# Kernel tuning notes

Measured on AMD Instinct MI355X. Metric: run time of the kernel, lower is better.

Reference implementation:

```python
import jax, jax.numpy as jnp
import numpy as np
from jax import lax

ALPHA = 0.99
EPS = 1e-14
B, C, T, F = 16, 2, 1000, 481


def setup_inputs() -> dict:
    key = jax.random.key(0)
    k1, _ = jax.random.split(key)
    x = jax.random.normal(k1, (B, C, T, F, 2), dtype=jnp.float32)
    init_state = jnp.ones((1, 1, F, 1), dtype=jnp.float32)
    return {"x": x, "init_state": init_state}


def reference(x, init_state):
    # complex path: x is [b, c, t, f, 2]
    b, c, t, f, _ = x.shape
    # magnitude per (b,c,t,f): sqrt(re^2 + im^2), clamped
    x_abs = jnp.sqrt(jnp.clip(jnp.sum(x * x, axis=-1, keepdims=True), EPS))  # [b,c,t,f,1]
    s0 = jnp.broadcast_to(init_state[:, :, :f], (b, c, f, 1))
    xs = jnp.moveaxis(x_abs, 2, 0)  # [t,b,c,f,1]

    def step(state, xa):
        state = xa * (1.0 - ALPHA) + state * ALPHA
        return state, state

    _, states = lax.scan(step, s0, xs)  # [t,b,c,f,1]
    states = jnp.moveaxis(states, 0, 2)  # [b,c,t,f,1]
    return x / jnp.sqrt(states)
```

## Files before the change

kernel.cpp:

```cpp
#include <hip/hip_runtime.h>


#define EPS_F 1e-14f

constexpr int B = 16, C = 2, T = 1000, F = 481;
constexpr int BC = B * C;
constexpr int FW = 64;
constexpr int NTILE = 8;
constexpr int WV = 8;
constexpr int RW = 25;
constexpr int RSTEP = WV * RW;
constexpr int NSUP = T / RSTEP;
constexpr int ROWS = F * 2;

__global__ __launch_bounds__(512, 4)
void k_fused(const float* __restrict__ x, const float* __restrict__ init_state,
             float* __restrict__ out) {
    __shared__ float lds_c[WV][FW];
    __shared__ float carry[FW];

    const int fx   = threadIdx.x & (FW - 1);
    const int w    = threadIdx.x >> 6;
    const int bc   = blockIdx.x & (BC - 1);
    const int tile = blockIdx.x >> 5;
    const int f    = tile * FW + fx;
    const bool act = (f < F);

    double p = 1.0;
    for (int i = 0; i < RW; ++i) p *= 0.99;
    const float A25 = (float)p;

    if (threadIdx.x < FW) carry[fx] = act ? init_state[f] : 1.0f;

    for (int s = 0; s < NSUP; ++s) {
        const int t0 = s * RSTEP + w * RW;
        const float* xp = x + ((size_t)(bc * T + t0) * F + f) * 2;

        float2 v[RW];
#pragma unroll
        for (int j = 0; j < RW; ++j)
            if (act) v[j] = *(const float2*)(xp + (size_t)j * ROWS);

        float Cl = 0.0f;
#pragma unroll
        for (int j = 0; j < RW; ++j)
            if (act) {
                float m = fmaxf(fmaf(v[j].x, v[j].x, v[j].y * v[j].y), EPS_F);
                Cl = fmaf(0.99f, Cl, 0.01f * __builtin_amdgcn_sqrtf(m));
            }
        lds_c[w][fx] = Cl;
        __syncthreads();

        float sloc = carry[fx];
#pragma unroll
        for (int jw = 0; jw < WV - 1; ++jw)
            if (jw < w) sloc = fmaf(A25, sloc, lds_c[jw][fx]);
        __syncthreads();

        if (w == WV - 1) carry[fx] = fmaf(A25, sloc, Cl);

        float* op = out + ((size_t)(bc * T + t0) * F + f) * 2;
#pragma unroll
        for (int j = 0; j < RW; ++j)
            if (act) {
                float m = fmaxf(fmaf(v[j].x, v[j].x, v[j].y * v[j].y), EPS_F);
                sloc = fmaf(0.99f, sloc, 0.01f * __builtin_amdgcn_sqrtf(m));
                const float inv = __builtin_amdgcn_rsqf(sloc);
                float2 o;
                o.x = v[j].x * inv;
                o.y = v[j].y * inv;
                *(float2*)(op + (size_t)j * ROWS) = o;
            }
    }
}

extern "C" void kernel_launch(void* const* d_in, const int* in_sizes, int n_in,
                              void* d_out, int out_size, void* d_ws, size_t ws_size,
                              hipStream_t stream) {
    const float* x          = (const float*)d_in[0];
    const float* init_state = (const float*)d_in[1];
    float* out = (float*)d_out;

    k_fused<<<dim3(NTILE * BC), 512, 0, stream>>>(x, init_state, out);
}
```

Baseline: 45.36 us.

## Split time scan across 16 waves in a single pass with re-read

Replaces the 5-iteration super-step loop with a single chunked scan where 16 waves each own about 62 consecutive time steps, combined via one LDS prefix using A62/A63 decay factors. Block size doubles to 1024 threads and only one barrier is needed. Inputs are no longer held in registers between the local-sum and output passes; they are re-read from memory, trading extra read traffic for fewer syncs and lower register pressure.

```diff
diff --git a/kernel.cpp b/kernel.cpp
--- a/kernel.cpp
+++ b/kernel.cpp
@@ -7,17 +7,18 @@
 constexpr int BC = B * C;
 constexpr int FW = 64;
 constexpr int NTILE = 8;
-constexpr int WV = 8;
-constexpr int RW = 25;
-constexpr int RSTEP = WV * RW;
-constexpr int NSUP = T / RSTEP;
+constexpr int WV = 16;
 constexpr int ROWS = F * 2;
 
-__global__ __launch_bounds__(512, 4)
+__device__ __forceinline__ int wbase(int w) {
+    return (w < 8) ? 63 * w : 504 + 62 * (w - 8);
+}
+__device__ __forceinline__ int wlen(int w) { return (w < 8) ? 63 : 62; }
+
+__global__ __launch_bounds__(1024, 4)
 void k_fused(const float* __restrict__ x, const float* __restrict__ init_state,
              float* __restrict__ out) {
     __shared__ float lds_c[WV][FW];
-    __shared__ float carry[FW];
 
     const int fx   = threadIdx.x & (FW - 1);
     const int w    = threadIdx.x >> 6;
@@ -27,50 +28,44 @@
     const bool act = (f < F);
 
     double p = 1.0;
-    for (int i = 0; i < RW; ++i) p *= 0.99;
-    const float A25 = (float)p;
+    for (int i = 0; i < 62; ++i) p *= 0.99;
+    const float A62 = (float)p;
+    const float A63 = (float)(p * 0.99);
 
-    if (threadIdx.x < FW) carry[fx] = act ? init_state[f] : 1.0f;
+    const int t0  = wbase(w);
+    const int len = wlen(w);
+    const float* xp = x + ((size_t)(bc * T + t0) * F + f) * 2;
 
-    for (int s = 0; s < NSUP; ++s) {
-        const int t0 = s * RSTEP + w * RW;
-        const float* xp = x + ((size_t)(bc * T + t0) * F + f) * 2;
+    float Cl = 0.0f;
+    if (act) {
+        for (int j = 0; j < len; ++j) {
+            float2 v = *(const float2*)(xp + (size_t)j * ROWS);
+            float m = fmaxf(fmaf(v.x, v.x, v.y * v.y), EPS_F);
+            Cl = fmaf(0.99f, Cl, 0.01f * __builtin_amdgcn_sqrtf(m));
+        }
+    }
+    lds_c[w][fx] = Cl;
+    __syncthreads();
 
-        float2 v[RW];
+    float sloc = act ? init_state[f] : 1.0f;
 #pragma unroll
-        for (int j = 0; j < RW; ++j)
-            if (act) v[j] = *(const float2*)(xp + (size_t)j * ROWS);
+    for (int jw = 0; jw < WV - 1; ++jw) {
+        const float aL = (jw < 8) ? A63 : A62;
+        if (jw < w) sloc = fmaf(aL, sloc, lds_c[jw][fx]);
+    }
 
-        float Cl = 0.0f;
-#pragma unroll
-        for (int j = 0; j < RW; ++j)
-            if (act) {
-                float m = fmaxf(fmaf(v[j].x, v[j].x, v[j].y * v[j].y), EPS_F);
-                Cl = fmaf(0.99f, Cl, 0.01f * __builtin_amdgcn_sqrtf(m));
-            }
-        lds_c[w][fx] = Cl;
-        __syncthreads();
-
-        float sloc = carry[fx];
-#pragma unroll
-        for (int jw = 0; jw < WV - 1; ++jw)
-            if (jw < w) sloc = fmaf(A25, sloc, lds_c[jw][fx]);
-        __syncthreads();
-
-        if (w == WV - 1) carry[fx] = fmaf(A25, sloc, Cl);
-
+    if (act) {
         float* op = out + ((size_t)(bc * T + t0) * F + f) * 2;
-#pragma unroll
-        for (int j = 0; j < RW; ++j)
-            if (act) {
-                float m = fmaxf(fmaf(v[j].x, v[j].x, v[j].y * v[j].y), EPS_F);
-                sloc = fmaf(0.99f, sloc, 0.01f * __builtin_amdgcn_sqrtf(m));
-                const float inv = __builtin_amdgcn_rsqf(sloc);
-                float2 o;
-                o.x = v[j].x * inv;
-                o.y = v[j].y * inv;
-                *(float2*)(op + (size_t)j * ROWS) = o;
-            }
+        for (int j = 0; j < len; ++j) {
+            float2 v = *(const float2*)(xp + (size_t)j * ROWS);
+            float m = fmaxf(fmaf(v.x, v.x, v.y * v.y), EPS_F);
+            sloc = fmaf(0.99f, sloc, 0.01f * __builtin_amdgcn_sqrtf(m));
+            const float inv = __builtin_amdgcn_rsqf(sloc);
+            float2 o;
+            o.x = v.x * inv;
+            o.y = v.y * inv;
+            *(float2*)(op + (size_t)j * ROWS) = o;
+        }
     }
 }
 
@@ -81,5 +76,5 @@
     const float* init_state = (const float*)d_in[1];
     float* out = (float*)d_out;
 
-    k_fused<<<dim3(NTILE * BC), 512, 0, stream>>>(x, init_state, out);
+    k_fused<<<dim3(NTILE * BC), 1024, 0, stream>>>(x, init_state, out);
 }
```

Result: slower. 62.23 us (+37.2%).

## Double-buffer superstep loads and prefetch next chunk during output pass

Applied to the files above, without the earlier changes.

Unrolls the five supersteps and keeps two register buffers, so the global loads for the next superstep are issued while the current one computes its outputs. Carry moves to a ping-pong pair in shared memory, and raw s_barrier plus waitcnt replace one of the two syncthreads. This is meant to hide global load latency behind compute. It raises register use, so launch bounds drop to 2 blocks per SM, which lowers occupancy.

```diff
diff --git a/kernel.cpp b/kernel.cpp
--- a/kernel.cpp
+++ b/kernel.cpp
@@ -13,11 +13,59 @@
 constexpr int NSUP = T / RSTEP;
 constexpr int ROWS = F * 2;
 
-__global__ __launch_bounds__(512, 4)
+#define LOADG(buf, sidx)                                                     \
+  {                                                                          \
+    const float* _xp = xp0 + (size_t)((sidx) * RSTEP) * ROWS;                \
+    _Pragma("unroll")                                                        \
+    for (int j = 0; j < RW; ++j)                                             \
+      (buf)[j] = act ? *(const float2*)(_xp + (size_t)j * ROWS)              \
+                     : make_float2(0.0f, 0.0f);                              \
+    _Pragma("unroll")                                                        \
+    for (int j = 0; j < RW; ++j)                                             \
+      asm volatile("" : "+v"((buf)[j].x), "+v"((buf)[j].y));                 \
+  }
+
+#define SUPERSTEP(sidx, cur, nxt, do_preload)                                \
+  {                                                                          \
+    float Cl = 0.0f;                                                         \
+    _Pragma("unroll")                                                        \
+    for (int j = 0; j < RW; ++j) {                                           \
+      float m = fmaxf(fmaf((cur)[j].x, (cur)[j].x, (cur)[j].y * (cur)[j].y), \
+                      EPS_F);                                                \
+      Cl = fmaf(0.99f, Cl, 0.01f * __builtin_amdgcn_sqrtf(m));               \
+    }                                                                        \
+    lds_c[w][fx] = Cl;                                                       \
+    asm volatile("s_waitcnt lgkmcnt(0)" ::: "memory");                       \
+    __builtin_amdgcn_s_barrier();                                            \
+    const int par = (sidx) & 1;                                              \
+    float sloc = carry[par][fx];                                             \
+    _Pragma("unroll")                                                        \
+    for (int jw = 0; jw < WV - 1; ++jw)                                      \
+      if (jw < w) sloc = fmaf(A25, sloc, lds_c[jw][fx]);                     \
+    if (w == WV - 1) carry[par ^ 1][fx] = fmaf(A25, sloc, Cl);               \
+    if (do_preload) LOADG(nxt, (sidx) + 1);                                  \
+    asm volatile("" ::: "memory");                                           \
+    float* _op = op0 + (size_t)((sidx) * RSTEP) * ROWS;                      \
+    _Pragma("unroll")                                                        \
+    for (int j = 0; j < RW; ++j) {                                           \
+      float2 v = (cur)[j];                                                   \
+      float m = fmaxf(fmaf(v.x, v.x, v.y * v.y), EPS_F);                     \
+      sloc = fmaf(0.99f, sloc, 0.01f * __builtin_amdgcn_sqrtf(m));           \
+      const float inv = __builtin_amdgcn_rsqf(sloc);                         \
+      float2 o;                                                              \
+      o.x = v.x * inv;                                                       \
+      o.y = v.y * inv;                                                       \
+      if (act) *(float2*)(_op + (size_t)j * ROWS) = o;                       \
+    }                                                                        \
+    asm volatile("s_waitcnt lgkmcnt(0)" ::: "memory");                       \
+    __builtin_amdgcn_s_barrier();                                            \
+  }
+
+__global__ __launch_bounds__(512, 2)
 void k_fused(const float* __restrict__ x, const float* __restrict__ init_state,
              float* __restrict__ out) {
     __shared__ float lds_c[WV][FW];
-    __shared__ float carry[FW];
+    __shared__ float carry[2][FW];
 
     const int fx   = threadIdx.x & (FW - 1);
     const int w    = threadIdx.x >> 6;
@@ -26,52 +74,23 @@
     const int f    = tile * FW + fx;
     const bool act = (f < F);
 
-    double p = 1.0;
-    for (int i = 0; i < RW; ++i) p *= 0.99;
-    const float A25 = (float)p;
+    double q = 1.0;
+    for (int i = 0; i < RW; ++i) q *= 0.99;
+    const float A25 = (float)q;
 
-    if (threadIdx.x < FW) carry[fx] = act ? init_state[f] : 1.0f;
+    if (threadIdx.x < FW) carry[0][fx] = act ? init_state[f] : 1.0f;
 
-    for (int s = 0; s < NSUP; ++s) {
-        const int t0 = s * RSTEP + w * RW;
-        const float* xp = x + ((size_t)(bc * T + t0) * F + f) * 2;
+    const float* xp0 = x   + ((size_t)(bc * T + w * RW) * F + f) * 2;
+    float*       op0 = out + ((size_t)(bc * T + w * RW) * F + f) * 2;
 
-        float2 v[RW];
-#pragma unroll
-        for (int j = 0; j < RW; ++j)
-            if (act) v[j] = *(const float2*)(xp + (size_t)j * ROWS);
+    float2 vA[RW], vB[RW];
 
-        float Cl = 0.0f;
-#pragma unroll
-        for (int j = 0; j < RW; ++j)
-            if (act) {
-                float m = fmaxf(fmaf(v[j].x, v[j].x, v[j].y * v[j].y), EPS_F);
-                Cl = fmaf(0.99f, Cl, 0.01f * __builtin_amdgcn_sqrtf(m));
-            }
-        lds_c[w][fx] = Cl;
-        __syncthreads();
-
-        float sloc = carry[fx];
-#pragma unroll
-        for (int jw = 0; jw < WV - 1; ++jw)
-            if (jw < w) sloc = fmaf(A25, sloc, lds_c[jw][fx]);
-        __syncthreads();
-
-        if (w == WV - 1) carry[fx] = fmaf(A25, sloc, Cl);
-
-        float* op = out + ((size_t)(bc * T + t0) * F + f) * 2;
-#pragma unroll
-        for (int j = 0; j < RW; ++j)
-            if (act) {
-                float m = fmaxf(fmaf(v[j].x, v[j].x, v[j].y * v[j].y), EPS_F);
-                sloc = fmaf(0.99f, sloc, 0.01f * __builtin_amdgcn_sqrtf(m));
-                const float inv = __builtin_amdgcn_rsqf(sloc);
-                float2 o;
-                o.x = v[j].x * inv;
-                o.y = v[j].y * inv;
-                *(float2*)(op + (size_t)j * ROWS) = o;
-            }
-    }
+    LOADG(vA, 0);
+    SUPERSTEP(0, vA, vB, true);
+    SUPERSTEP(1, vB, vA, true);
+    SUPERSTEP(2, vA, vB, true);
+    SUPERSTEP(3, vB, vA, true);
+    SUPERSTEP(4, vA, vB, false);
 }
 
 extern "C" void kernel_launch(void* const* d_in, const int* in_sizes, int n_in,
```

Measured after the change: 41.98 us. 1.08x faster.
